# Kernel optimization log

Hardware: AMD Instinct MI355X
Metric: run time of the kernel (lower is better)

Reference implementation:

```python
import jax, jax.numpy as jnp
import numpy as np

T, B, D = 2048, 32, 1024
AH, H = 128, 8
N, N2 = D // H, AH // H


def setup_inputs() -> dict:
    key = jax.random.key(0)
    ks = jax.random.split(key, 7)
    s1 = 1.0 / np.sqrt(N)
    s2 = 1.0 / np.sqrt(N2)
    return {
        "hyp": jax.random.normal(ks[0], (T, B, D), dtype=jnp.float32),
        "W_w": jax.random.uniform(ks[1], (N2, N), jnp.float32, -s1, s1),
        "W_b": jax.random.uniform(ks[2], (N2,), jnp.float32, -s1, s1),
        "Wm_w": jax.random.uniform(ks[3], (N2, N), jnp.float32, -s1, s1),
        "Wm_b": jax.random.uniform(ks[4], (N2,), jnp.float32, -s1, s1),
        "Wh_w": jax.random.uniform(ks[5], (1, N2), jnp.float32, -s2, s2),
        "Wh_b": jax.random.uniform(ks[6], (1,), jnp.float32, -s2, s2),
        "dan_hidden_size": D,
        "attention_hidden_size": AH,
        "multihead_size": H,
    }


def reference(hyp, W_w, W_b, Wm_w, Wm_b, Wh_w, Wh_b,
              dan_hidden_size, attention_hidden_size, multihead_size):
    t, b, d = hyp.shape
    h_ = multihead_size
    n = d // h_
    # (T,B,D) -> (B,H,T,N); weights are shared across heads in the original loop
    x = jnp.transpose(hyp.reshape(t, b, h_, n), (1, 2, 0, 3))
    m = x.mean(axis=2, keepdims=True)                      # (B,H,1,N) mean over time
    gate_x = jnp.tanh(jnp.einsum('bhtn,kn->bhtk', x, W_w) + W_b)
    gate_m = jnp.tanh(jnp.einsum('bhtn,kn->bhtk', m, Wm_w) + Wm_b)
    hgate = gate_x * gate_m                                 # (B,H,T,N2)
    logits = jnp.einsum('bhtk,ok->bhto', hgate, Wh_w) + Wh_b  # (B,H,T,1)
    a = jax.nn.softmax(logits, axis=2)                      # softmax over time
    c = jnp.sum(a * x, axis=2)                              # (B,H,N)
    return c.reshape(b, h_ * n)
```

## Files before the change

kernel.cpp:

```cpp
#include <hip/hip_runtime.h>
#include <math.h>

#define T_   2048
#define B_   32
#define D_   1024
#define H_   8
#define N_   128
#define NK   16
#define TSPL 8
#define TBLK (T_/TSPL)
#define BD   (B_*D_)
#define BD4  (BD/4)
#define APS  132
#define LOG2E 1.4426950408889634f

typedef __attribute__((ext_vector_type(8))) short short8;
typedef __attribute__((ext_vector_type(4))) float f32x4;

__device__ __forceinline__ void split_bf16(float4 a, float4 b,
                                           short8& hi, short8& lo) {
    union { uint32_t u[4]; short8 v; } H, L;
    uint32_t x0 = __float_as_uint(a.x), x1 = __float_as_uint(a.y);
    uint32_t x2 = __float_as_uint(a.z), x3 = __float_as_uint(a.w);
    uint32_t x4 = __float_as_uint(b.x), x5 = __float_as_uint(b.y);
    uint32_t x6 = __float_as_uint(b.z), x7 = __float_as_uint(b.w);
    H.u[0] = (x0 >> 16) | (x1 & 0xFFFF0000u);
    H.u[1] = (x2 >> 16) | (x3 & 0xFFFF0000u);
    H.u[2] = (x4 >> 16) | (x5 & 0xFFFF0000u);
    H.u[3] = (x6 >> 16) | (x7 & 0xFFFF0000u);
    float l0 = a.x - __uint_as_float(x0 & 0xFFFF0000u);
    float l1 = a.y - __uint_as_float(x1 & 0xFFFF0000u);
    float l2 = a.z - __uint_as_float(x2 & 0xFFFF0000u);
    float l3 = a.w - __uint_as_float(x3 & 0xFFFF0000u);
    float l4 = b.x - __uint_as_float(x4 & 0xFFFF0000u);
    float l5 = b.y - __uint_as_float(x5 & 0xFFFF0000u);
    float l6 = b.z - __uint_as_float(x6 & 0xFFFF0000u);
    float l7 = b.w - __uint_as_float(x7 & 0xFFFF0000u);
    L.u[0] = (__float_as_uint(l0) >> 16) | (__float_as_uint(l1) & 0xFFFF0000u);
    L.u[1] = (__float_as_uint(l2) >> 16) | (__float_as_uint(l3) & 0xFFFF0000u);
    L.u[2] = (__float_as_uint(l4) >> 16) | (__float_as_uint(l5) & 0xFFFF0000u);
    L.u[3] = (__float_as_uint(l6) >> 16) | (__float_as_uint(l7) & 0xFFFF0000u);
    hi = H.v; lo = L.v;
}

__device__ __forceinline__ float tanh_fast(float d) {
    return 1.f - 2.f * __frcp_rn(exp2f(d * (2.f * LOG2E)) + 1.f);
}

#define LOADX(dst, step_) { \
    const int trow_ = t0 + (step_) * 64 + w * 16 + kk; \
    const size_t rb_ = (size_t)trow_ * BD4 + base4; \
    (dst)[0] = hyp4[rb_ + g * 2];      (dst)[1] = hyp4[rb_ + g * 2 + 1]; \
    (dst)[2] = hyp4[rb_ + 8 + g * 2];  (dst)[3] = hyp4[rb_ + 8 + g * 2 + 1]; \
    (dst)[4] = hyp4[rb_ + 16 + g * 2]; (dst)[5] = hyp4[rb_ + 16 + g * 2 + 1]; \
    (dst)[6] = hyp4[rb_ + 24 + g * 2]; (dst)[7] = hyp4[rb_ + 24 + g * 2 + 1]; }

__global__ __launch_bounds__(256, 2) void k_p(const float* __restrict__ hyp,
                                              const float* __restrict__ Ww,
                                              const float* __restrict__ Wb,
                                              float* __restrict__ part,
                                              float* __restrict__ Pbuf) {
    __shared__ float red[4 * N_];
    const int tid  = threadIdx.x;
    const int lane = tid & 63;
    const int w    = tid >> 6;
    const int blk  = blockIdx.x;
    const int bh   = blk >> 3;
    const int spl  = blk & 7;
    const int b = bh >> 3, h = bh & 7;
    const int t0 = spl * TBLK;
    const float4* hyp4 = (const float4*)hyp;
    const float4* Ww4  = (const float4*)Ww;
    const int base4 = b * (D_ / 4) + h * (N_ / 4);
    const int kk = lane & 15;
    const int g  = lane >> 4;

    short8 wh[4], wl[4];
#pragma unroll
    for (int ks = 0; ks < 4; ++ks) {
        float4 wa  = Ww4[kk * 32 + ks * 8 + g * 2];
        float4 wb4 = Ww4[kk * 32 + ks * 8 + g * 2 + 1];
        split_bf16(wa, wb4, wh[ks], wl[ks]);
    }
    const float wbr = Wb[kk];

    float4 cs[8];
#pragma unroll
    for (int m = 0; m < 8; ++m) cs[m] = make_float4(0.f, 0.f, 0.f, 0.f);

    float4 xq[2][8];
    LOADX(xq[0], 0);
#pragma unroll
    for (int step = 0; step < 4; ++step) {
        const int cur = step & 1, nxt = cur ^ 1;
        if (step < 3) LOADX(xq[nxt], step + 1);
#pragma unroll
        for (int m = 0; m < 8; ++m) {
            cs[m].x += xq[cur][m].x; cs[m].y += xq[cur][m].y;
            cs[m].z += xq[cur][m].z; cs[m].w += xq[cur][m].w;
        }
        f32x4 acc = {0.f, 0.f, 0.f, 0.f};
#pragma unroll
        for (int ks = 0; ks < 4; ++ks) {
            short8 xh, xl;
            split_bf16(xq[cur][2*ks], xq[cur][2*ks+1], xh, xl);
            acc = __builtin_amdgcn_mfma_f32_16x16x32_bf16(xh, wh[ks], acc, 0, 0, 0);
            acc = __builtin_amdgcn_mfma_f32_16x16x32_bf16(xl, wh[ks], acc, 0, 0, 0);
            acc = __builtin_amdgcn_mfma_f32_16x16x32_bf16(xh, wl[ks], acc, 0, 0, 0);
        }
        const int tl = t0 + step * 64 + w * 16 + g * 4;
        const size_t pb = ((size_t)bh * T_ + tl) * NK + kk;
#pragma unroll
        for (int i = 0; i < 4; ++i)
            Pbuf[pb + (size_t)i * NK] = tanh_fast(acc[i] + wbr);
    }
#pragma unroll
    for (int m = 0; m < 8; ++m) {
#pragma unroll
        for (int mask = 1; mask <= 8; mask <<= 1) {
            cs[m].x += __shfl_xor(cs[m].x, mask, 64);
            cs[m].y += __shfl_xor(cs[m].y, mask, 64);
            cs[m].z += __shfl_xor(cs[m].z, mask, 64);
            cs[m].w += __shfl_xor(cs[m].w, mask, 64);
        }
    }
    if (kk == 0) {
#pragma unroll
        for (int m = 0; m < 8; ++m) {
            int nb = 32 * (m >> 1) + 8 * g + 4 * (m & 1);
            red[w * N_ + nb + 0] = cs[m].x;
            red[w * N_ + nb + 1] = cs[m].y;
            red[w * N_ + nb + 2] = cs[m].z;
            red[w * N_ + nb + 3] = cs[m].w;
        }
    }
    __syncthreads();
    if (tid < N_)
        part[blk * N_ + tid] = (red[tid] + red[N_ + tid])
                             + (red[2*N_ + tid] + red[3*N_ + tid]);
}

__global__ __launch_bounds__(256, 2) void k_att(const float* __restrict__ hyp,
                                                const float* __restrict__ part,
                                                const float* __restrict__ Wmw,
                                                const float* __restrict__ Wmb,
                                                const float* __restrict__ Whw,
                                                const float* __restrict__ Pbuf,
                                                float* __restrict__ attp) {
    __shared__ float red[4 * N_];
    __shared__ float zred[4];
    __shared__ float m_l[N_];
    __shared__ float gw_l[NK];
    const int tid  = threadIdx.x;
    const int lane = tid & 63;
    const int w    = tid >> 6;
    const int blk  = (B_ * H_ * TSPL - 1) - (int)blockIdx.x;
    const int bh   = blk >> 3;
    const int spl  = blk & 7;
    const int b = bh >> 3, h = bh & 7;
    const int t0 = spl * TBLK;
    const float4* hyp4  = (const float4*)hyp;
    const float4* Pbuf4 = (const float4*)Pbuf;
    const int base4 = b * (D_ / 4) + h * (N_ / 4);
    const int kk = lane & 15;
    const int g  = lane >> 4;

    if (tid < N_) {
        float s = 0.f;
#pragma unroll
        for (int s8 = 0; s8 < TSPL; ++s8) s += part[(bh * TSPL + s8) * N_ + tid];
        m_l[tid] = s * (1.f / (float)T_);
    }
    __syncthreads();
    if (tid < N_) {
        int k = tid >> 3, g3 = tid & 7;
        float dsum = 0.f;
#pragma unroll
        for (int i = 0; i < 16; ++i) {
            int n = g3 * 16 + i;
            dsum = fmaf(m_l[n], Wmw[k * N_ + n], dsum);
        }
        dsum += __shfl_xor(dsum, 1, 64);
        dsum += __shfl_xor(dsum, 2, 64);
        dsum += __shfl_xor(dsum, 4, 64);
        if (g3 == 0) gw_l[k] = tanhf(dsum + Wmb[k]) * Whw[k];
    }
    __syncthreads();
    float gmv[NK];
#pragma unroll
    for (int j = 0; j < NK; ++j) gmv[j] = gw_l[j];

    float4 xq[2][8], pr[2][4];
    LOADX(xq[0], 0);
    {
        const int trow_ = t0 + w * 16 + kk;
        const size_t pb_ = (size_t)(bh * T_ + trow_) * 4;
        pr[0][0] = Pbuf4[pb_];     pr[0][1] = Pbuf4[pb_ + 1];
        pr[0][2] = Pbuf4[pb_ + 2]; pr[0][3] = Pbuf4[pb_ + 3];
    }
    float4 cacc[8];
#pragma unroll
    for (int m = 0; m < 8; ++m) cacc[m] = make_float4(0.f, 0.f, 0.f, 0.f);
    float zacc = 0.f;

#pragma unroll
    for (int step = 0; step < 4; ++step) {
        const int cur = step & 1, nxt = cur ^ 1;
        if (step < 3) {
            LOADX(xq[nxt], step + 1);
            const int trow_ = t0 + (step + 1) * 64 + w * 16 + kk;
            const size_t pb_ = (size_t)(bh * T_ + trow_) * 4;
            pr[nxt][0] = Pbuf4[pb_];     pr[nxt][1] = Pbuf4[pb_ + 1];
            pr[nxt][2] = Pbuf4[pb_ + 2]; pr[nxt][3] = Pbuf4[pb_ + 3];
        }
        float lg = 0.f;
#pragma unroll
        for (int q = 0; q < 4; ++q) {
            lg = fmaf(pr[cur][q].x, gmv[4*q + 0], lg);
            lg = fmaf(pr[cur][q].y, gmv[4*q + 1], lg);
            lg = fmaf(pr[cur][q].z, gmv[4*q + 2], lg);
            lg = fmaf(pr[cur][q].w, gmv[4*q + 3], lg);
        }
        float e = exp2f(lg * LOG2E);
        zacc += e;
#pragma unroll
        for (int m = 0; m < 8; ++m) {
            cacc[m].x = fmaf(e, xq[cur][m].x, cacc[m].x);
            cacc[m].y = fmaf(e, xq[cur][m].y, cacc[m].y);
            cacc[m].z = fmaf(e, xq[cur][m].z, cacc[m].z);
            cacc[m].w = fmaf(e, xq[cur][m].w, cacc[m].w);
        }
    }
#pragma unroll
    for (int m = 0; m < 8; ++m) {
#pragma unroll
        for (int mask = 1; mask <= 8; mask <<= 1) {
            cacc[m].x += __shfl_xor(cacc[m].x, mask, 64);
            cacc[m].y += __shfl_xor(cacc[m].y, mask, 64);
            cacc[m].z += __shfl_xor(cacc[m].z, mask, 64);
            cacc[m].w += __shfl_xor(cacc[m].w, mask, 64);
        }
    }
    float z = zacc;
    z += __shfl_xor(z, 1, 64);
    z += __shfl_xor(z, 2, 64);
    z += __shfl_xor(z, 4, 64);
    z += __shfl_xor(z, 8, 64);
    if (kk == 0) {
#pragma unroll
        for (int m = 0; m < 8; ++m) {
            int nb = 32 * (m >> 1) + 8 * g + 4 * (m & 1);
            red[w * N_ + nb + 0] = cacc[m].x;
            red[w * N_ + nb + 1] = cacc[m].y;
            red[w * N_ + nb + 2] = cacc[m].z;
            red[w * N_ + nb + 3] = cacc[m].w;
        }
    }
    if (lane == 0) zred[w] = z;
    __syncthreads();
    if (tid < N_) {
        attp[(size_t)blk * APS + tid] =
            (red[tid] + red[N_ + tid]) + (red[2*N_ + tid] + red[3*N_ + tid]);
    } else if (tid == N_) {
        attp[(size_t)blk * APS + N_] =
            (zred[0] + zred[1]) + (zred[2] + zred[3]);
    }
}

__global__ __launch_bounds__(128) void k_red(const float* __restrict__ attp,
                                             float* __restrict__ out) {
    int bh = blockIdx.x, tid = threadIdx.x;
    float Z = 0.f, c = 0.f;
#pragma unroll
    for (int s = 0; s < TSPL; ++s) {
        const float* pp = &attp[(size_t)(bh * TSPL + s) * APS];
        Z += pp[N_];
        c += pp[tid];
    }
    out[bh * N_ + tid] = c / Z;
}

extern "C" void kernel_launch(void* const* d_in, const int* in_sizes, int n_in,
                              void* d_out, int out_size, void* d_ws, size_t ws_size,
                              hipStream_t stream) {
    const float* hyp = (const float*)d_in[0];
    const float* Ww  = (const float*)d_in[1];
    const float* Wb  = (const float*)d_in[2];
    const float* Wmw = (const float*)d_in[3];
    const float* Wmb = (const float*)d_in[4];
    const float* Whw = (const float*)d_in[5];
    float* out  = (float*)d_out;
    float* part = (float*)d_ws;
    float* attp = part + 2048 * N_;
    float* Pbuf = part + (1 << 20);

    k_p  <<<dim3(B_ * H_ * TSPL), 256, 0, stream>>>(hyp, Ww, Wb, part, Pbuf);
    k_att<<<dim3(B_ * H_ * TSPL), 256, 0, stream>>>(hyp, part, Wmw, Wmb, Whw,
                                                    Pbuf, attp);
    k_red<<<dim3(B_ * H_), 128, 0, stream>>>(attp, out);
}
```

Measured before the change: 111.1 us.

## Fuse projection, attention and reduction into one per-head kernel with LDS gate buffer

Replaces the three-kernel pipeline (gate projection, attention pass, final reduction) with a single kernel where one 512-thread block owns a whole (batch, head) pair over all 2048 timesteps. The tanh gate values are kept in a padded shared-memory buffer instead of a global scratch buffer, and the time-mean and softmax normalisation are reduced inside the block. This removes the global Pbuf round trip, the partial-sum buffers and two kernel launches. The cost is a very large LDS footprint that limits each CU to one block, and only 256 blocks across the device, which reduces latency hiding while hyp is still streamed twice.

```diff
diff --git a/kernel.cpp b/kernel.cpp
--- a/kernel.cpp
+++ b/kernel.cpp
@@ -7,11 +7,8 @@
 #define H_   8
 #define N_   128
 #define NK   16
-#define TSPL 8
-#define TBLK (T_/TSPL)
-#define BD   (B_*D_)
-#define BD4  (BD/4)
-#define APS  132
+#define BD4  (B_*D_/4)
+#define PST  18
 #define LOG2E 1.4426950408889634f
 
 typedef __attribute__((ext_vector_type(8))) short short8;
@@ -47,53 +44,54 @@
     return 1.f - 2.f * __frcp_rn(exp2f(d * (2.f * LOG2E)) + 1.f);
 }
 
-#define LOADX(dst, step_) { \
-    const int trow_ = t0 + (step_) * 64 + w * 16 + kk; \
+#define LOADX(dst, s_) { \
+    const int trow_ = (s_) * 128 + w * 16 + kk; \
     const size_t rb_ = (size_t)trow_ * BD4 + base4; \
     (dst)[0] = hyp4[rb_ + g * 2];      (dst)[1] = hyp4[rb_ + g * 2 + 1]; \
     (dst)[2] = hyp4[rb_ + 8 + g * 2];  (dst)[3] = hyp4[rb_ + 8 + g * 2 + 1]; \
     (dst)[4] = hyp4[rb_ + 16 + g * 2]; (dst)[5] = hyp4[rb_ + 16 + g * 2 + 1]; \
     (dst)[6] = hyp4[rb_ + 24 + g * 2]; (dst)[7] = hyp4[rb_ + 24 + g * 2 + 1]; }
 
-__global__ __launch_bounds__(256, 2) void k_p(const float* __restrict__ hyp,
-                                              const float* __restrict__ Ww,
-                                              const float* __restrict__ Wb,
-                                              float* __restrict__ part,
-                                              float* __restrict__ Pbuf) {
-    __shared__ float red[4 * N_];
+__global__ __launch_bounds__(512, 2) void k_fused(
+        const float* __restrict__ hyp,  const float* __restrict__ Ww,
+        const float* __restrict__ Wb,   const float* __restrict__ Wmw,
+        const float* __restrict__ Wmb,  const float* __restrict__ Whw,
+        float* __restrict__ out) {
+    __shared__ float Pl[T_ * PST];
+    __shared__ float red[8 * N_];
+    __shared__ float m_l[N_];
+    __shared__ float gw_l[NK];
+    __shared__ float zred[8];
+
     const int tid  = threadIdx.x;
     const int lane = tid & 63;
     const int w    = tid >> 6;
-    const int blk  = blockIdx.x;
-    const int bh   = blk >> 3;
-    const int spl  = blk & 7;
+    const int bh   = blockIdx.x;
     const int b = bh >> 3, h = bh & 7;
-    const int t0 = spl * TBLK;
     const float4* hyp4 = (const float4*)hyp;
     const float4* Ww4  = (const float4*)Ww;
     const int base4 = b * (D_ / 4) + h * (N_ / 4);
     const int kk = lane & 15;
     const int g  = lane >> 4;
 
-    short8 wh[4], wl[4];
+    short8 wh[4], wlo[4];
 #pragma unroll
     for (int ks = 0; ks < 4; ++ks) {
         float4 wa  = Ww4[kk * 32 + ks * 8 + g * 2];
         float4 wb4 = Ww4[kk * 32 + ks * 8 + g * 2 + 1];
-        split_bf16(wa, wb4, wh[ks], wl[ks]);
+        split_bf16(wa, wb4, wh[ks], wlo[ks]);
     }
     const float wbr = Wb[kk];
 
     float4 cs[8];
 #pragma unroll
     for (int m = 0; m < 8; ++m) cs[m] = make_float4(0.f, 0.f, 0.f, 0.f);
-
     float4 xq[2][8];
     LOADX(xq[0], 0);
 #pragma unroll
-    for (int step = 0; step < 4; ++step) {
-        const int cur = step & 1, nxt = cur ^ 1;
-        if (step < 3) LOADX(xq[nxt], step + 1);
+    for (int s = 0; s < 16; ++s) {
+        const int cur = s & 1, nxt = cur ^ 1;
+        if (s < 15) LOADX(xq[nxt], s + 1);
 #pragma unroll
         for (int m = 0; m < 8; ++m) {
             cs[m].x += xq[cur][m].x; cs[m].y += xq[cur][m].y;
@@ -104,15 +102,14 @@
         for (int ks = 0; ks < 4; ++ks) {
             short8 xh, xl;
             split_bf16(xq[cur][2*ks], xq[cur][2*ks+1], xh, xl);
-            acc = __builtin_amdgcn_mfma_f32_16x16x32_bf16(xh, wh[ks], acc, 0, 0, 0);
-            acc = __builtin_amdgcn_mfma_f32_16x16x32_bf16(xl, wh[ks], acc, 0, 0, 0);
-            acc = __builtin_amdgcn_mfma_f32_16x16x32_bf16(xh, wl[ks], acc, 0, 0, 0);
-        }
-        const int tl = t0 + step * 64 + w * 16 + g * 4;
-        const size_t pb = ((size_t)bh * T_ + tl) * NK + kk;
+            acc = __builtin_amdgcn_mfma_f32_16x16x32_bf16(xh, wh[ks],  acc, 0, 0, 0);
+            acc = __builtin_amdgcn_mfma_f32_16x16x32_bf16(xl, wh[ks],  acc, 0, 0, 0);
+            acc = __builtin_amdgcn_mfma_f32_16x16x32_bf16(xh, wlo[ks], acc, 0, 0, 0);
+        }
+        const int tl = s * 128 + w * 16 + g * 4;
 #pragma unroll
         for (int i = 0; i < 4; ++i)
-            Pbuf[pb + (size_t)i * NK] = tanh_fast(acc[i] + wbr);
+            Pl[(tl + i) * PST + kk] = tanh_fast(acc[i] + wbr);
     }
 #pragma unroll
     for (int m = 0; m < 8; ++m) {
@@ -135,40 +132,10 @@
         }
     }
     __syncthreads();
-    if (tid < N_)
-        part[blk * N_ + tid] = (red[tid] + red[N_ + tid])
-                             + (red[2*N_ + tid] + red[3*N_ + tid]);
-}
-
-__global__ __launch_bounds__(256, 2) void k_att(const float* __restrict__ hyp,
-                                                const float* __restrict__ part,
-                                                const float* __restrict__ Wmw,
-                                                const float* __restrict__ Wmb,
-                                                const float* __restrict__ Whw,
-                                                const float* __restrict__ Pbuf,
-                                                float* __restrict__ attp) {
-    __shared__ float red[4 * N_];
-    __shared__ float zred[4];
-    __shared__ float m_l[N_];
-    __shared__ float gw_l[NK];
-    const int tid  = threadIdx.x;
-    const int lane = tid & 63;
-    const int w    = tid >> 6;
-    const int blk  = (B_ * H_ * TSPL - 1) - (int)blockIdx.x;
-    const int bh   = blk >> 3;
-    const int spl  = blk & 7;
-    const int b = bh >> 3, h = bh & 7;
-    const int t0 = spl * TBLK;
-    const float4* hyp4  = (const float4*)hyp;
-    const float4* Pbuf4 = (const float4*)Pbuf;
-    const int base4 = b * (D_ / 4) + h * (N_ / 4);
-    const int kk = lane & 15;
-    const int g  = lane >> 4;
-
     if (tid < N_) {
         float s = 0.f;
 #pragma unroll
-        for (int s8 = 0; s8 < TSPL; ++s8) s += part[(bh * TSPL + s8) * N_ + tid];
+        for (int w8 = 0; w8 < 8; ++w8) s += red[w8 * N_ + tid];
         m_l[tid] = s * (1.f / (float)T_);
     }
     __syncthreads();
@@ -190,36 +157,23 @@
 #pragma unroll
     for (int j = 0; j < NK; ++j) gmv[j] = gw_l[j];
 
-    float4 xq[2][8], pr[2][4];
-    LOADX(xq[0], 0);
-    {
-        const int trow_ = t0 + w * 16 + kk;
-        const size_t pb_ = (size_t)(bh * T_ + trow_) * 4;
-        pr[0][0] = Pbuf4[pb_];     pr[0][1] = Pbuf4[pb_ + 1];
-        pr[0][2] = Pbuf4[pb_ + 2]; pr[0][3] = Pbuf4[pb_ + 3];
-    }
     float4 cacc[8];
 #pragma unroll
     for (int m = 0; m < 8; ++m) cacc[m] = make_float4(0.f, 0.f, 0.f, 0.f);
     float zacc = 0.f;
-
-#pragma unroll
-    for (int step = 0; step < 4; ++step) {
-        const int cur = step & 1, nxt = cur ^ 1;
-        if (step < 3) {
-            LOADX(xq[nxt], step + 1);
-            const int trow_ = t0 + (step + 1) * 64 + w * 16 + kk;
-            const size_t pb_ = (size_t)(bh * T_ + trow_) * 4;
-            pr[nxt][0] = Pbuf4[pb_];     pr[nxt][1] = Pbuf4[pb_ + 1];
-            pr[nxt][2] = Pbuf4[pb_ + 2]; pr[nxt][3] = Pbuf4[pb_ + 3];
-        }
+    LOADX(xq[0], 0);
+#pragma unroll
+    for (int s = 0; s < 16; ++s) {
+        const int cur = s & 1, nxt = cur ^ 1;
+        if (s < 15) LOADX(xq[nxt], s + 1);
+        const int tr = s * 128 + w * 16 + kk;
+        const float2* prow = (const float2*)&Pl[tr * PST];
         float lg = 0.f;
 #pragma unroll
-        for (int q = 0; q < 4; ++q) {
-            lg = fmaf(pr[cur][q].x, gmv[4*q + 0], lg);
-            lg = fmaf(pr[cur][q].y, gmv[4*q + 1], lg);
-            lg = fmaf(pr[cur][q].z, gmv[4*q + 2], lg);
-            lg = fmaf(pr[cur][q].w, gmv[4*q + 3], lg);
+        for (int q = 0; q < 8; ++q) {
+            float2 pv = prow[q];
+            lg = fmaf(pv.x, gmv[2*q + 0], lg);
+            lg = fmaf(pv.y, gmv[2*q + 1], lg);
         }
         float e = exp2f(lg * LOG2E);
         zacc += e;
@@ -259,25 +213,13 @@
     if (lane == 0) zred[w] = z;
     __syncthreads();
     if (tid < N_) {
-        attp[(size_t)blk * APS + tid] =
-            (red[tid] + red[N_ + tid]) + (red[2*N_ + tid] + red[3*N_ + tid]);
-    } else if (tid == N_) {
-        attp[(size_t)blk * APS + N_] =
-            (zred[0] + zred[1]) + (zred[2] + zred[3]);
-    }
-}
-
-__global__ __launch_bounds__(128) void k_red(const float* __restrict__ attp,
-                                             float* __restrict__ out) {
-    int bh = blockIdx.x, tid = threadIdx.x;
-    float Z = 0.f, c = 0.f;
-#pragma unroll
-    for (int s = 0; s < TSPL; ++s) {
-        const float* pp = &attp[(size_t)(bh * TSPL + s) * APS];
-        Z += pp[N_];
-        c += pp[tid];
-    }
-    out[bh * N_ + tid] = c / Z;
+        float Z = ((zred[0] + zred[1]) + (zred[2] + zred[3]))
+                + ((zred[4] + zred[5]) + (zred[6] + zred[7]));
+        float c = 0.f;
+#pragma unroll
+        for (int w8 = 0; w8 < 8; ++w8) c += red[w8 * N_ + tid];
+        out[bh * N_ + tid] = c / Z;
+    }
 }
 
 extern "C" void kernel_launch(void* const* d_in, const int* in_sizes, int n_in,
@@ -289,13 +231,7 @@
     const float* Wmw = (const float*)d_in[3];
     const float* Wmb = (const float*)d_in[4];
     const float* Whw = (const float*)d_in[5];
-    float* out  = (float*)d_out;
-    float* part = (float*)d_ws;
-    float* attp = part + 2048 * N_;
-    float* Pbuf = part + (1 << 20);
-
-    k_p  <<<dim3(B_ * H_ * TSPL), 256, 0, stream>>>(hyp, Ww, Wb, part, Pbuf);
-    k_att<<<dim3(B_ * H_ * TSPL), 256, 0, stream>>>(hyp, part, Wmw, Wmb, Whw,
-                                                    Pbuf, attp);
-    k_red<<<dim3(B_ * H_), 128, 0, stream>>>(attp, out);
-}
+    float* out = (float*)d_out;
+
+    k_fused<<<dim3(B_ * H_), 512, 0, stream>>>(hyp, Ww, Wb, Wmw, Wmb, Whw, out);
+}
```

Measured after the change: 127.2 us. +14.5%, slower.

## Store gate intermediates as fp16, drop register double-buffering, raise occupancy

Applied to the files above, without the earlier changes.

Stores the tanh gate buffer in half precision instead of fp32, which halves its write and read traffic between the two kernels. The explicit register double-buffering of hyp and Pbuf loads is removed so the loops load per step. Launch bounds go from 2 to 4 waves per SIMD, so latency hiding comes from more resident waves instead of software prefetch. This trades some precision in the logits, and a tighter register budget could cause spills.

```diff
diff --git a/kernel.cpp b/kernel.cpp
--- a/kernel.cpp
+++ b/kernel.cpp
@@ -1,4 +1,5 @@
 #include <hip/hip_runtime.h>
+#include <hip/hip_fp16.h>
 #include <math.h>
 
 #define T_   2048
@@ -9,8 +10,7 @@
 #define NK   16
 #define TSPL 8
 #define TBLK (T_/TSPL)
-#define BD   (B_*D_)
-#define BD4  (BD/4)
+#define BD4  (B_*D_/4)
 #define APS  132
 #define LOG2E 1.4426950408889634f
 
@@ -55,11 +55,11 @@
     (dst)[4] = hyp4[rb_ + 16 + g * 2]; (dst)[5] = hyp4[rb_ + 16 + g * 2 + 1]; \
     (dst)[6] = hyp4[rb_ + 24 + g * 2]; (dst)[7] = hyp4[rb_ + 24 + g * 2 + 1]; }
 
-__global__ __launch_bounds__(256, 2) void k_p(const float* __restrict__ hyp,
+__global__ __launch_bounds__(256, 4) void k_p(const float* __restrict__ hyp,
                                               const float* __restrict__ Ww,
                                               const float* __restrict__ Wb,
                                               float* __restrict__ part,
-                                              float* __restrict__ Pbuf) {
+                                              __half* __restrict__ Pbuf) {
     __shared__ float red[4 * N_];
     const int tid  = threadIdx.x;
     const int lane = tid & 63;
@@ -75,12 +75,12 @@
     const int kk = lane & 15;
     const int g  = lane >> 4;
 
-    short8 wh[4], wl[4];
+    short8 wh[4], wlo[4];
 #pragma unroll
     for (int ks = 0; ks < 4; ++ks) {
         float4 wa  = Ww4[kk * 32 + ks * 8 + g * 2];
         float4 wb4 = Ww4[kk * 32 + ks * 8 + g * 2 + 1];
-        split_bf16(wa, wb4, wh[ks], wl[ks]);
+        split_bf16(wa, wb4, wh[ks], wlo[ks]);
     }
     const float wbr = Wb[kk];
 
@@ -88,31 +88,29 @@
 #pragma unroll
     for (int m = 0; m < 8; ++m) cs[m] = make_float4(0.f, 0.f, 0.f, 0.f);
 
-    float4 xq[2][8];
-    LOADX(xq[0], 0);
 #pragma unroll
     for (int step = 0; step < 4; ++step) {
-        const int cur = step & 1, nxt = cur ^ 1;
-        if (step < 3) LOADX(xq[nxt], step + 1);
-#pragma unroll
-        for (int m = 0; m < 8; ++m) {
-            cs[m].x += xq[cur][m].x; cs[m].y += xq[cur][m].y;
-            cs[m].z += xq[cur][m].z; cs[m].w += xq[cur][m].w;
+        float4 xq[8];
+        LOADX(xq, step);
+#pragma unroll
+        for (int m = 0; m < 8; ++m) {
+            cs[m].x += xq[m].x; cs[m].y += xq[m].y;
+            cs[m].z += xq[m].z; cs[m].w += xq[m].w;
         }
         f32x4 acc = {0.f, 0.f, 0.f, 0.f};
 #pragma unroll
         for (int ks = 0; ks < 4; ++ks) {
             short8 xh, xl;
-            split_bf16(xq[cur][2*ks], xq[cur][2*ks+1], xh, xl);
-            acc = __builtin_amdgcn_mfma_f32_16x16x32_bf16(xh, wh[ks], acc, 0, 0, 0);
-            acc = __builtin_amdgcn_mfma_f32_16x16x32_bf16(xl, wh[ks], acc, 0, 0, 0);
-            acc = __builtin_amdgcn_mfma_f32_16x16x32_bf16(xh, wl[ks], acc, 0, 0, 0);
+            split_bf16(xq[2*ks], xq[2*ks+1], xh, xl);
+            acc = __builtin_amdgcn_mfma_f32_16x16x32_bf16(xh, wh[ks],  acc, 0, 0, 0);
+            acc = __builtin_amdgcn_mfma_f32_16x16x32_bf16(xl, wh[ks],  acc, 0, 0, 0);
+            acc = __builtin_amdgcn_mfma_f32_16x16x32_bf16(xh, wlo[ks], acc, 0, 0, 0);
         }
         const int tl = t0 + step * 64 + w * 16 + g * 4;
         const size_t pb = ((size_t)bh * T_ + tl) * NK + kk;
 #pragma unroll
         for (int i = 0; i < 4; ++i)
-            Pbuf[pb + (size_t)i * NK] = tanh_fast(acc[i] + wbr);
+            Pbuf[pb + (size_t)i * NK] = __float2half(tanh_fast(acc[i] + wbr));
     }
 #pragma unroll
     for (int m = 0; m < 8; ++m) {
@@ -140,12 +138,12 @@
                              + (red[2*N_ + tid] + red[3*N_ + tid]);
 }
 
-__global__ __launch_bounds__(256, 2) void k_att(const float* __restrict__ hyp,
+__global__ __launch_bounds__(256, 4) void k_att(const float* __restrict__ hyp,
                                                 const float* __restrict__ part,
                                                 const float* __restrict__ Wmw,
                                                 const float* __restrict__ Wmb,
                                                 const float* __restrict__ Whw,
-                                                const float* __restrict__ Pbuf,
+                                                const __half* __restrict__ Pbuf,
                                                 float* __restrict__ attp) {
     __shared__ float red[4 * N_];
     __shared__ float zred[4];
@@ -159,8 +157,7 @@
     const int spl  = blk & 7;
     const int b = bh >> 3, h = bh & 7;
     const int t0 = spl * TBLK;
-    const float4* hyp4  = (const float4*)hyp;
-    const float4* Pbuf4 = (const float4*)Pbuf;
+    const float4* hyp4 = (const float4*)hyp;
     const int base4 = b * (D_ / 4) + h * (N_ / 4);
     const int kk = lane & 15;
     const int g  = lane >> 4;
@@ -190,14 +187,6 @@
 #pragma unroll
     for (int j = 0; j < NK; ++j) gmv[j] = gw_l[j];
 
-    float4 xq[2][8], pr[2][4];
-    LOADX(xq[0], 0);
-    {
-        const int trow_ = t0 + w * 16 + kk;
-        const size_t pb_ = (size_t)(bh * T_ + trow_) * 4;
-        pr[0][0] = Pbuf4[pb_];     pr[0][1] = Pbuf4[pb_ + 1];
-        pr[0][2] = Pbuf4[pb_ + 2]; pr[0][3] = Pbuf4[pb_ + 3];
-    }
     float4 cacc[8];
 #pragma unroll
     for (int m = 0; m < 8; ++m) cacc[m] = make_float4(0.f, 0.f, 0.f, 0.f);
@@ -205,30 +194,30 @@
 
 #pragma unroll
     for (int step = 0; step < 4; ++step) {
-        const int cur = step & 1, nxt = cur ^ 1;
-        if (step < 3) {
-            LOADX(xq[nxt], step + 1);
-            const int trow_ = t0 + (step + 1) * 64 + w * 16 + kk;
-            const size_t pb_ = (size_t)(bh * T_ + trow_) * 4;
-            pr[nxt][0] = Pbuf4[pb_];     pr[nxt][1] = Pbuf4[pb_ + 1];
-            pr[nxt][2] = Pbuf4[pb_ + 2]; pr[nxt][3] = Pbuf4[pb_ + 3];
-        }
+        const int tr = t0 + step * 64 + w * 16 + kk;
+        union { uint4 u; __half2 h[8]; } P0, P1;
+        const uint4* pv = (const uint4*)(Pbuf + (size_t)(bh * T_ + tr) * NK);
+        P0.u = pv[0]; P1.u = pv[1];
+        float4 xq[8];
+        LOADX(xq, step);
         float lg = 0.f;
 #pragma unroll
         for (int q = 0; q < 4; ++q) {
-            lg = fmaf(pr[cur][q].x, gmv[4*q + 0], lg);
-            lg = fmaf(pr[cur][q].y, gmv[4*q + 1], lg);
-            lg = fmaf(pr[cur][q].z, gmv[4*q + 2], lg);
-            lg = fmaf(pr[cur][q].w, gmv[4*q + 3], lg);
+            float2 f0 = __half22float2(P0.h[q]);
+            float2 f1 = __half22float2(P1.h[q]);
+            lg = fmaf(f0.x, gmv[2*q + 0], lg);
+            lg = fmaf(f0.y, gmv[2*q + 1], lg);
+            lg = fmaf(f1.x, gmv[8 + 2*q + 0], lg);
+            lg = fmaf(f1.y, gmv[8 + 2*q + 1], lg);
         }
         float e = exp2f(lg * LOG2E);
         zacc += e;
 #pragma unroll
         for (int m = 0; m < 8; ++m) {
-            cacc[m].x = fmaf(e, xq[cur][m].x, cacc[m].x);
-            cacc[m].y = fmaf(e, xq[cur][m].y, cacc[m].y);
-            cacc[m].z = fmaf(e, xq[cur][m].z, cacc[m].z);
-            cacc[m].w = fmaf(e, xq[cur][m].w, cacc[m].w);
+            cacc[m].x = fmaf(e, xq[m].x, cacc[m].x);
+            cacc[m].y = fmaf(e, xq[m].y, cacc[m].y);
+            cacc[m].z = fmaf(e, xq[m].z, cacc[m].z);
+            cacc[m].w = fmaf(e, xq[m].w, cacc[m].w);
         }
     }
 #pragma unroll
@@ -292,7 +281,7 @@
     float* out  = (float*)d_out;
     float* part = (float*)d_ws;
     float* attp = part + 2048 * N_;
-    float* Pbuf = part + (1 << 20);
+    __half* Pbuf = (__half*)((char*)d_ws + (4 << 20));
 
     k_p  <<<dim3(B_ * H_ * TSPL), 256, 0, stream>>>(hyp, Ww, Wb, part, Pbuf);
     k_att<<<dim3(B_ * H_ * TSPL), 256, 0, stream>>>(hyp, part, Wmw, Wmb, Whw,
```

After: 106.1 us. -4.5%, faster.
